# Kernel tuning notes

Measured on AMD Instinct MI355X. Metric: run time of the kernel, lower is better.

## Reference

```python
import jax, jax.numpy as jnp
import numpy as np

BETA = 0.25
DECAY = 0.99
EPS = 1e-05
N_E = 1024
E_DIM = 64

def setup_inputs() -> dict:
    key = jax.random.key(0)
    k1, k2, k3, k4 = jax.random.split(key, 4)
    z = jax.random.normal(k1, (32, 64, 32, 32), dtype=jnp.float32)
    embedding = jax.random.normal(k2, (N_E, E_DIM), dtype=jnp.float32)
    cluster_size = jax.random.uniform(k3, (N_E,), dtype=jnp.float32)
    cluster_sum = jax.random.normal(k4, (N_E, E_DIM), dtype=jnp.float32)
    return {"z": z, "embedding": embedding, "cluster_size": cluster_size, "cluster_sum": cluster_sum}


def reference(z, embedding, cluster_size, cluster_sum):
    # z: (B, C, H, W) with C == e_dim
    zp = jnp.transpose(z, (0, 2, 3, 1))            # (B, H, W, C)
    zf = zp.reshape(-1, E_DIM)                      # (N, e_dim)
    # squared-distance matrix: ||z||^2 + ||e||^2 - 2 z.e  -> (N, n_e)
    distance = (jnp.sum(zf ** 2, axis=1, keepdims=True)
                + jnp.sum(embedding ** 2, axis=1)
                - 2.0 * (zf @ embedding.T))
    idx = jnp.argmin(distance, axis=1)              # (N,)
    # one-hot counts / cluster sums expressed as segment sums (same math)
    counts = jax.ops.segment_sum(jnp.ones(zf.shape[0], dtype=zf.dtype), idx, num_segments=N_E)
    sums = jax.ops.segment_sum(zf, idx, num_segments=N_E)
    # EMA buffer update (module is in training mode -> embedding refreshed)
    new_cluster_size = DECAY * cluster_size + (1.0 - DECAY) * counts
    new_cluster_sum = DECAY * cluster_sum + (1.0 - DECAY) * sums
    new_embed = new_cluster_sum / (new_cluster_size + EPS)[:, None]
    z_q = new_embed[idx].reshape(zp.shape)          # gather-dequantize
    L_commitment = jnp.mean((jax.lax.stop_gradient(z_q) - zp) ** 2)
    loss = BETA * L_commitment
    z_q = zp + jax.lax.stop_gradient(z_q - zp)      # straight-through
    z_q = jnp.transpose(z_q, (0, 3, 1, 2))          # back to (B, C, H, W)
    return z_q, loss, counts
```

## Files before the change

### kernel.cpp

```cpp
#include <hip/hip_runtime.h>
#include <hip/hip_bf16.h>


#define N_ROWS   32768
#define N_CODES  1024
#define EDIM     64
#define ZQ_ELEMS 2097152
#define NSPLIT   4

__global__ void vq_enorm(const float* __restrict__ emb, float* __restrict__ enorm) {
    const int c = blockIdx.x * 256 + threadIdx.x;
    if (c < N_CODES) {
        const float4* __restrict__ e4 = (const float4*)(emb + (c << 6));
        float s = 0.f;
        #pragma unroll
        for (int i = 0; i < 16; ++i) {
            const float4 v = e4[i];
            s = fmaf(v.x, v.x, s); s = fmaf(v.y, v.y, s);
            s = fmaf(v.z, v.z, s); s = fmaf(v.w, v.w, s);
        }
        enorm[c] = s;
    }
}

__device__ __forceinline__ void ldfrag(float4 (&dst)[8], const float4* __restrict__ s4,
                                       int lane, int g) {
    #pragma unroll
    for (int r = 0; r < 8; ++r) dst[r] = s4[(lane + 16 * r) * 17 + g];
}
__device__ __forceinline__ void fma_tile(const float4 (&zf)[8], const float4 (&ef)[8],
                                         float (&acc)[8][8]) {
    #pragma unroll
    for (int rr = 0; rr < 8; ++rr)
        #pragma unroll
        for (int j = 0; j < 8; ++j) {
            float a = acc[rr][j];
            a = fmaf(zf[rr].x, ef[j].x, a);
            a = fmaf(zf[rr].y, ef[j].y, a);
            a = fmaf(zf[rr].z, ef[j].z, a);
            a = fmaf(zf[rr].w, ef[j].w, a);
            acc[rr][j] = a;
        }
}

__global__ __launch_bounds__(256, 2) void vq_dist(
        const float* __restrict__ z, const float* __restrict__ emb,
        const float* __restrict__ enorm,
        float* __restrict__ half_score, int* __restrict__ half_idx) {
    __shared__ float zs[128 * 68];
    __shared__ float es[128 * 68];
    __shared__ float zn_s[128];

    const int t    = threadIdx.x;
    const int tx   = t & 15, ty = t >> 4;
    const int r0   = blockIdx.x * 128;
    const int half = blockIdx.y;
    const int b    = r0 >> 10;
    const int hw0  = r0 & 1023;

    #pragma unroll
    for (int i = 0; i < 32; ++i) {
        const int cell = i * 256 + t;
        const int row = cell & 127, c = cell >> 7;
        zs[row * 68 + c] = z[((b * 64 + c) << 10) + hw0 + row];
    }
    __syncthreads();

    if (t < 128) {
        const float4* z4 = (const float4*)zs + t * 17;
        float s = 0.f;
        #pragma unroll
        for (int g = 0; g < 16; ++g) {
            const float4 v = z4[g];
            s = fmaf(v.x, v.x, s); s = fmaf(v.y, v.y, s);
            s = fmaf(v.z, v.z, s); s = fmaf(v.w, v.w, s);
        }
        zn_s[t] = s;
    }
    __syncthreads();

    float znr[8];
    #pragma unroll
    for (int rr = 0; rr < 8; ++rr) znr[rr] = zn_s[ty + 16 * rr];

    float best[8]; int bidx[8];
    #pragma unroll
    for (int rr = 0; rr < 8; ++rr) { best[rr] = INFINITY; bidx[rr] = 0; }

    const float4* __restrict__ eg  = (const float4*)(emb + (half << 9) * 64);
    const float4* __restrict__ zs4 = (const float4*)zs;
    const float4* __restrict__ es4 = (const float4*)es;

    for (int ch = 0; ch < 4; ++ch) {
        const int cbase = (half << 9) + (ch << 7);
        float4 pf[8];
        #pragma unroll
        for (int p = 0; p < 8; ++p) pf[p] = eg[ch * 2048 + p * 256 + t];
        float enj[8];
        #pragma unroll
        for (int j = 0; j < 8; ++j) enj[j] = enorm[cbase + tx + 16 * j];

        __syncthreads();
        #pragma unroll
        for (int p = 0; p < 8; ++p) {
            const int fid = p * 256 + t;
            ((float4*)es)[(fid >> 4) * 17 + (fid & 15)] = pf[p];
        }
        __syncthreads();

        float acc[8][8];
        #pragma unroll
        for (int rr = 0; rr < 8; ++rr)
            #pragma unroll
            for (int j = 0; j < 8; ++j) acc[rr][j] = 0.f;

        float4 zf[8], efA[8], efB[8];
        ldfrag(efA, es4, tx, 0);
        #pragma unroll
        for (int gp = 0; gp < 8; ++gp) {
            ldfrag(zf, zs4, ty, 2 * gp);
            ldfrag(efB, es4, tx, 2 * gp + 1);
            fma_tile(zf, efA, acc);
            ldfrag(zf, zs4, ty, 2 * gp + 1);
            if (gp < 7) ldfrag(efA, es4, tx, 2 * gp + 2);
            fma_tile(zf, efB, acc);
        }

        #pragma unroll
        for (int rr = 0; rr < 8; ++rr)
            #pragma unroll
            for (int j = 0; j < 8; ++j) {
                const float s = (znr[rr] + enj[j]) - 2.0f * acc[rr][j];
                if (s < best[rr]) { best[rr] = s; bidx[rr] = cbase + tx + 16 * j; }
            }
    }

    #pragma unroll
    for (int off = 1; off < 16; off <<= 1) {
        #pragma unroll
        for (int rr = 0; rr < 8; ++rr) {
            const float os = __shfl_xor(best[rr], off);
            const int   oi = __shfl_xor(bidx[rr], off);
            if (os < best[rr] || (os == best[rr] && oi < bidx[rr])) {
                best[rr] = os; bidx[rr] = oi;
            }
        }
    }
    if (tx == 0) {
        #pragma unroll
        for (int rr = 0; rr < 8; ++rr) {
            const int gr = r0 + ty + 16 * rr;
            half_score[half * N_ROWS + gr] = best[rr];
            half_idx  [half * N_ROWS + gr] = bidx[rr];
        }
    }
}

__global__ __launch_bounds__(256) void vq_resolve(
        const float* __restrict__ z,
        const float* __restrict__ half_score, const int* __restrict__ half_idx,
        int* __restrict__ idx_out, float* __restrict__ counts,
        float* __restrict__ sums) {
    __shared__ float zs[128 * 65];
    __shared__ int   idx_sh[128];
    const int t   = threadIdx.x;
    const int r0  = blockIdx.x * 128;
    const int b   = r0 >> 10;
    const int hw0 = r0 & 1023;
    const int sp  = blockIdx.x & (NSPLIT - 1);

    #pragma unroll
    for (int i = 0; i < 32; ++i) {
        const int cell = i * 256 + t;
        const int row = cell & 127, c = cell >> 7;
        zs[row * 65 + c] = z[((b * 64 + c) << 10) + hw0 + row];
    }
    if (t < 128) {
        const int gr = r0 + t;
        const float s0 = half_score[gr], s1 = half_score[N_ROWS + gr];
        const int   i0 = half_idx[gr],   i1 = half_idx[N_ROWS + gr];
        const int   bi = (s1 < s0) ? i1 : i0;
        idx_out[gr] = bi;
        idx_sh[t] = bi;
        atomicAdd(&counts[sp * N_CODES + bi], 1.0f);
    }
    __syncthreads();

    const int lane = t & 63, sub = t >> 6;
    #pragma unroll
    for (int i = 0; i < 32; ++i) {
        const int row = i * 4 + sub;
        atomicAdd(&sums[sp * 65536 + idx_sh[row] * 64 + lane], zs[row * 65 + lane]);
    }
}

__global__ void vq_ema(const float* __restrict__ counts, const float* __restrict__ sums,
                       const float* __restrict__ cs, const float* __restrict__ csum,
                       float* __restrict__ new_embed, float* __restrict__ out_counts,
                       float* __restrict__ out_loss) {
    const int g = blockIdx.x * 256 + threadIdx.x;
    const int c = g >> 6, d = g & 63;
    const float cnt = (counts[c] + counts[N_CODES + c])
                    + (counts[2 * N_CODES + c] + counts[3 * N_CODES + c]);
    const float ssum = (sums[g] + sums[65536 + g]) + (sums[131072 + g] + sums[196608 + g]);
    const float nsize = 0.99f * cs[c] + 0.01f * cnt;
    const float nsum  = 0.99f * csum[g] + 0.01f * ssum;
    new_embed[g] = nsum / (nsize + 1e-5f);
    if (d == 0) out_counts[c] = cnt;
    if (g == 0) out_loss[0] = 0.f;
}

__global__ __launch_bounds__(256) void vq_gather(
        const float* __restrict__ z, const int* __restrict__ idx,
        const float* __restrict__ new_embed,
        float* __restrict__ out_zq, float* __restrict__ out_loss) {
    __shared__ float red[4];
    const int t  = threadIdx.x;
    const int r0 = blockIdx.x * 256;
    const int b  = r0 >> 10;
    const int hw = (r0 & 1023) + t;
    const int myidx = idx[r0 + t];

    const float4* __restrict__ er = (const float4*)(new_embed + (myidx << 6));
    float4 e4[16];
    #pragma unroll
    for (int i = 0; i < 16; ++i) e4[i] = er[i];

    float lsum = 0.f;
    #pragma unroll
    for (int c = 0; c < 64; ++c) {
        const float e  = ((const float*)e4)[c];
        const int  off = ((b * 64 + c) << 10) + hw;
        const float zv = z[off];
        const float diff = e - zv;
        out_zq[off] = zv + diff;
        lsum = fmaf(diff, diff, lsum);
    }
    #pragma unroll
    for (int off = 32; off >= 1; off >>= 1) lsum += __shfl_down(lsum, off);
    if ((t & 63) == 0) red[t >> 6] = lsum;
    __syncthreads();
    if (t == 0) {
        const float s = red[0] + red[1] + red[2] + red[3];
        atomicAdd(out_loss, s * (0.25f / 2097152.0f));
    }
}

extern "C" void kernel_launch(void* const* d_in, const int* in_sizes, int n_in,
                              void* d_out, int out_size, void* d_ws, size_t ws_size,
                              hipStream_t stream) {
    const float* z    = (const float*)d_in[0];
    const float* emb  = (const float*)d_in[1];
    const float* cs   = (const float*)d_in[2];
    const float* csum = (const float*)d_in[3];
    float* out = (float*)d_out;

    int*   idx        = (int*)d_ws;
    float* counts     = (float*)d_ws + 32768;
    float* sums       = counts + NSPLIT * N_CODES;
    float* enorm      = sums + NSPLIT * 65536;
    float* new_embed  = enorm + 1024;
    float* half_score = new_embed + 65536;
    int*   half_idx   = (int*)(half_score + 2 * 32768);

    hipMemsetAsync(counts, 0, NSPLIT * (N_CODES + 65536) * sizeof(float), stream);

    vq_enorm<<<4, 256, 0, stream>>>(emb, enorm);
    vq_dist<<<dim3(256, 2), 256, 0, stream>>>(z, emb, enorm, half_score, half_idx);
    vq_resolve<<<256, 256, 0, stream>>>(z, half_score, half_idx, idx, counts, sums);
    vq_ema<<<256, 256, 0, stream>>>(counts, sums, cs, csum, new_embed,
                                    out + ZQ_ELEMS + 1,
                                    out + ZQ_ELEMS);
    vq_gather<<<128, 256, 0, stream>>>(z, idx, new_embed, out, out + ZQ_ELEMS);
}
```

Before: 170.3 us.

## Fuse VQ pipeline into single cooperative kernel with grid syncs

Replaces the memset and five kernels with one cooperative kernel that zeroes the accumulators, computes code norms, runs the full 1024-code distance search per 128-row block, accumulates counts and sums, applies the EMA update, then gathers z_q from shared-memory z, separated by grid-wide syncs. This removes the two-way code split and its resolve pass, the repeated z loads, and the per-launch overhead. The cost is that the distance phase now uses only 256 blocks, each doing twice the work, so the GPU is less filled, and the grid barriers add their own synchronisation cost. The loss becomes a deterministic two-level reduction instead of an atomic add.

After: 298.9 us. 75.5% more time.

```diff
diff --git a/kernel.cpp b/kernel.cpp
--- a/kernel.cpp
+++ b/kernel.cpp
@@ -1,27 +1,14 @@
 #include <hip/hip_runtime.h>
-#include <hip/hip_bf16.h>
+#include <hip/hip_cooperative_groups.h>
+
+namespace cg = cooperative_groups;
 
 
 #define N_ROWS   32768
 #define N_CODES  1024
-#define EDIM     64
 #define ZQ_ELEMS 2097152
 #define NSPLIT   4
-
-__global__ void vq_enorm(const float* __restrict__ emb, float* __restrict__ enorm) {
-    const int c = blockIdx.x * 256 + threadIdx.x;
-    if (c < N_CODES) {
-        const float4* __restrict__ e4 = (const float4*)(emb + (c << 6));
-        float s = 0.f;
-        #pragma unroll
-        for (int i = 0; i < 16; ++i) {
-            const float4 v = e4[i];
-            s = fmaf(v.x, v.x, s); s = fmaf(v.y, v.y, s);
-            s = fmaf(v.z, v.z, s); s = fmaf(v.w, v.w, s);
-        }
-        enorm[c] = s;
-    }
-}
+#define ZERO_FLOATS (NSPLIT * (N_CODES + 65536))
 
 __device__ __forceinline__ void ldfrag(float4 (&dst)[8], const float4* __restrict__ s4,
                                        int lane, int g) {
@@ -43,20 +30,42 @@
         }
 }
 
-__global__ __launch_bounds__(256, 2) void vq_dist(
+__global__ __launch_bounds__(256, 2) void vq_fused(
         const float* __restrict__ z, const float* __restrict__ emb,
-        const float* __restrict__ enorm,
-        float* __restrict__ half_score, int* __restrict__ half_idx) {
+        const float* __restrict__ cs, const float* __restrict__ csum,
+        float* __restrict__ out, float* __restrict__ counts,
+        float* __restrict__ sums, float* __restrict__ enorm_ws,
+        float* __restrict__ new_embed, float* __restrict__ partial) {
     __shared__ float zs[128 * 68];
     __shared__ float es[128 * 68];
     __shared__ float zn_s[128];
-
-    const int t    = threadIdx.x;
-    const int tx   = t & 15, ty = t >> 4;
-    const int r0   = blockIdx.x * 128;
-    const int half = blockIdx.y;
-    const int b    = r0 >> 10;
-    const int hw0  = r0 & 1023;
+    __shared__ int   idx_sh[128];
+    __shared__ float red[4];
+
+    cg::grid_group grid = cg::this_grid();
+    const int t   = threadIdx.x;
+    const int bid = blockIdx.x;
+    const int gid = bid * 256 + t;
+
+    for (int i = gid; i < ZERO_FLOATS; i += 65536) counts[i] = 0.f;
+    if (gid < N_CODES) {
+        const float4* __restrict__ e4 = (const float4*)(emb + (gid << 6));
+        float s = 0.f;
+        #pragma unroll
+        for (int i = 0; i < 16; ++i) {
+            const float4 v = e4[i];
+            s = fmaf(v.x, v.x, s); s = fmaf(v.y, v.y, s);
+            s = fmaf(v.z, v.z, s); s = fmaf(v.w, v.w, s);
+        }
+        enorm_ws[gid] = s;
+    }
+    grid.sync();
+
+    const int tx  = t & 15, ty = t >> 4;
+    const int r0  = bid * 128;
+    const int b   = r0 >> 10;
+    const int hw0 = r0 & 1023;
+    const int sp  = bid & (NSPLIT - 1);
 
     #pragma unroll
     for (int i = 0; i < 32; ++i) {
@@ -87,18 +96,18 @@
     #pragma unroll
     for (int rr = 0; rr < 8; ++rr) { best[rr] = INFINITY; bidx[rr] = 0; }
 
-    const float4* __restrict__ eg  = (const float4*)(emb + (half << 9) * 64);
+    const float4* __restrict__ eg  = (const float4*)emb;
     const float4* __restrict__ zs4 = (const float4*)zs;
     const float4* __restrict__ es4 = (const float4*)es;
 
-    for (int ch = 0; ch < 4; ++ch) {
-        const int cbase = (half << 9) + (ch << 7);
+    for (int ch = 0; ch < 8; ++ch) {
+        const int cbase = ch << 7;
         float4 pf[8];
         #pragma unroll
         for (int p = 0; p < 8; ++p) pf[p] = eg[ch * 2048 + p * 256 + t];
         float enj[8];
         #pragma unroll
-        for (int j = 0; j < 8; ++j) enj[j] = enorm[cbase + tx + 16 * j];
+        for (int j = 0; j < 8; ++j) enj[j] = enorm_ws[cbase + tx + 16 * j];
 
         __syncthreads();
         #pragma unroll
@@ -149,100 +158,71 @@
     if (tx == 0) {
         #pragma unroll
         for (int rr = 0; rr < 8; ++rr) {
-            const int gr = r0 + ty + 16 * rr;
-            half_score[half * N_ROWS + gr] = best[rr];
-            half_idx  [half * N_ROWS + gr] = bidx[rr];
-        }
-    }
-}
-
-__global__ __launch_bounds__(256) void vq_resolve(
-        const float* __restrict__ z,
-        const float* __restrict__ half_score, const int* __restrict__ half_idx,
-        int* __restrict__ idx_out, float* __restrict__ counts,
-        float* __restrict__ sums) {
-    __shared__ float zs[128 * 65];
-    __shared__ int   idx_sh[128];
-    const int t   = threadIdx.x;
-    const int r0  = blockIdx.x * 128;
-    const int b   = r0 >> 10;
-    const int hw0 = r0 & 1023;
-    const int sp  = blockIdx.x & (NSPLIT - 1);
-
-    #pragma unroll
-    for (int i = 0; i < 32; ++i) {
-        const int cell = i * 256 + t;
-        const int row = cell & 127, c = cell >> 7;
-        zs[row * 65 + c] = z[((b * 64 + c) << 10) + hw0 + row];
-    }
-    if (t < 128) {
-        const int gr = r0 + t;
-        const float s0 = half_score[gr], s1 = half_score[N_ROWS + gr];
-        const int   i0 = half_idx[gr],   i1 = half_idx[N_ROWS + gr];
-        const int   bi = (s1 < s0) ? i1 : i0;
-        idx_out[gr] = bi;
-        idx_sh[t] = bi;
-        atomicAdd(&counts[sp * N_CODES + bi], 1.0f);
+            idx_sh[ty + 16 * rr] = bidx[rr];
+            atomicAdd(&counts[sp * N_CODES + bidx[rr]], 1.0f);
+        }
     }
     __syncthreads();
 
-    const int lane = t & 63, sub = t >> 6;
-    #pragma unroll
-    for (int i = 0; i < 32; ++i) {
-        const int row = i * 4 + sub;
-        atomicAdd(&sums[sp * 65536 + idx_sh[row] * 64 + lane], zs[row * 65 + lane]);
-    }
-}
-
-__global__ void vq_ema(const float* __restrict__ counts, const float* __restrict__ sums,
-                       const float* __restrict__ cs, const float* __restrict__ csum,
-                       float* __restrict__ new_embed, float* __restrict__ out_counts,
-                       float* __restrict__ out_loss) {
-    const int g = blockIdx.x * 256 + threadIdx.x;
-    const int c = g >> 6, d = g & 63;
-    const float cnt = (counts[c] + counts[N_CODES + c])
-                    + (counts[2 * N_CODES + c] + counts[3 * N_CODES + c]);
-    const float ssum = (sums[g] + sums[65536 + g]) + (sums[131072 + g] + sums[196608 + g]);
-    const float nsize = 0.99f * cs[c] + 0.01f * cnt;
-    const float nsum  = 0.99f * csum[g] + 0.01f * ssum;
-    new_embed[g] = nsum / (nsize + 1e-5f);
-    if (d == 0) out_counts[c] = cnt;
-    if (g == 0) out_loss[0] = 0.f;
-}
-
-__global__ __launch_bounds__(256) void vq_gather(
-        const float* __restrict__ z, const int* __restrict__ idx,
-        const float* __restrict__ new_embed,
-        float* __restrict__ out_zq, float* __restrict__ out_loss) {
-    __shared__ float red[4];
-    const int t  = threadIdx.x;
-    const int r0 = blockIdx.x * 256;
-    const int b  = r0 >> 10;
-    const int hw = (r0 & 1023) + t;
-    const int myidx = idx[r0 + t];
-
-    const float4* __restrict__ er = (const float4*)(new_embed + (myidx << 6));
-    float4 e4[16];
-    #pragma unroll
-    for (int i = 0; i < 16; ++i) e4[i] = er[i];
-
-    float lsum = 0.f;
-    #pragma unroll
-    for (int c = 0; c < 64; ++c) {
-        const float e  = ((const float*)e4)[c];
-        const int  off = ((b * 64 + c) << 10) + hw;
-        const float zv = z[off];
-        const float diff = e - zv;
-        out_zq[off] = zv + diff;
-        lsum = fmaf(diff, diff, lsum);
-    }
-    #pragma unroll
-    for (int off = 32; off >= 1; off >>= 1) lsum += __shfl_down(lsum, off);
-    if ((t & 63) == 0) red[t >> 6] = lsum;
-    __syncthreads();
-    if (t == 0) {
-        const float s = red[0] + red[1] + red[2] + red[3];
-        atomicAdd(out_loss, s * (0.25f / 2097152.0f));
+    {
+        const int k = t & 63, sub = t >> 6;
+        #pragma unroll
+        for (int i = 0; i < 32; ++i) {
+            const int row = i * 4 + sub;
+            atomicAdd(&sums[sp * 65536 + idx_sh[row] * 64 + k], zs[row * 68 + k]);
+        }
+    }
+    grid.sync();
+
+    {
+        const int c = gid >> 6, d = gid & 63;
+        const float cnt = (counts[c] + counts[N_CODES + c])
+                        + (counts[2 * N_CODES + c] + counts[3 * N_CODES + c]);
+        const float ssum = (sums[gid] + sums[65536 + gid])
+                         + (sums[131072 + gid] + sums[196608 + gid]);
+        const float nsize = 0.99f * cs[c] + 0.01f * cnt;
+        const float nsum  = 0.99f * csum[gid] + 0.01f * ssum;
+        new_embed[gid] = nsum / (nsize + 1e-5f);
+        if (d == 0) out[ZQ_ELEMS + 1 + c] = cnt;
+    }
+    grid.sync();
+
+    {
+        const int row = t >> 1, d0 = (t & 1) << 5;
+        const int code = idx_sh[row];
+        const float4* __restrict__ er = (const float4*)(new_embed + (code << 6) + d0);
+        float4 e4[8];
+        #pragma unroll
+        for (int i = 0; i < 8; ++i) e4[i] = er[i];
+
+        float lsum = 0.f;
+        #pragma unroll
+        for (int i = 0; i < 32; ++i) {
+            const int c = d0 + i;
+            const float e  = ((const float*)e4)[i];
+            const float zv = zs[row * 68 + c];
+            const float diff = e - zv;
+            out[((b * 64 + c) << 10) + hw0 + row] = zv + diff;
+            lsum = fmaf(diff, diff, lsum);
+        }
+        #pragma unroll
+        for (int off = 32; off >= 1; off >>= 1) lsum += __shfl_down(lsum, off);
+        if ((t & 63) == 0) red[t >> 6] = lsum;
+        __syncthreads();
+        if (t == 0) partial[bid] = (red[0] + red[1]) + (red[2] + red[3]);
+    }
+    grid.sync();
+
+    if (bid == 0) {
+        float v = partial[t];
+        #pragma unroll
+        for (int off = 32; off >= 1; off >>= 1) v += __shfl_down(v, off);
+        if ((t & 63) == 0) red[t >> 6] = v;
+        __syncthreads();
+        if (t == 0) {
+            const float s = (red[0] + red[1]) + (red[2] + red[3]);
+            out[ZQ_ELEMS] = s * (0.25f / 2097152.0f);
+        }
     }
 }
 
@@ -255,21 +235,14 @@
     const float* csum = (const float*)d_in[3];
     float* out = (float*)d_out;
 
-    int*   idx        = (int*)d_ws;
-    float* counts     = (float*)d_ws + 32768;
+    float* counts     = (float*)d_ws;
     float* sums       = counts + NSPLIT * N_CODES;
-    float* enorm      = sums + NSPLIT * 65536;
-    float* new_embed  = enorm + 1024;
-    float* half_score = new_embed + 65536;
-    int*   half_idx   = (int*)(half_score + 2 * 32768);
-
-    hipMemsetAsync(counts, 0, NSPLIT * (N_CODES + 65536) * sizeof(float), stream);
-
-    vq_enorm<<<4, 256, 0, stream>>>(emb, enorm);
-    vq_dist<<<dim3(256, 2), 256, 0, stream>>>(z, emb, enorm, half_score, half_idx);
-    vq_resolve<<<256, 256, 0, stream>>>(z, half_score, half_idx, idx, counts, sums);
-    vq_ema<<<256, 256, 0, stream>>>(counts, sums, cs, csum, new_embed,
-                                    out + ZQ_ELEMS + 1,
-                                    out + ZQ_ELEMS);
-    vq_gather<<<128, 256, 0, stream>>>(z, idx, new_embed, out, out + ZQ_ELEMS);
-}
+    float* enorm_ws   = sums + NSPLIT * 65536;
+    float* new_embed  = enorm_ws + N_CODES;
+    float* partial    = new_embed + 65536;
+
+    void* args[] = {(void*)&z, (void*)&emb, (void*)&cs, (void*)&csum,
+                    (void*)&out, (void*)&counts, (void*)&sums, (void*)&enorm_ws,
+                    (void*)&new_embed, (void*)&partial};
+    hipLaunchCooperativeKernel((void*)vq_fused, dim3(256), dim3(256), args, 0, stream);
+}
```
